# Performance work log

Hardware: AMD Instinct MI355X
Metric: run time of the kernel (lower is better)

Reference implementation:

```python
import jax, jax.numpy as jnp
import numpy as np

B, T, V, D, SLOTS = 16, 4096, 32000, 512, 256
EPS = 1e-5


def setup_inputs() -> dict:
    key = jax.random.key(0)
    ks = jax.random.split(key, 12)
    s = 0.02
    return {
        "seq": jax.random.randint(ks[0], (B, T), 0, V),
        "emb": jax.random.normal(ks[1], (V, D), jnp.float32) * s,
        "w1": jax.random.normal(ks[2], (D, 2 * D), jnp.float32) * s,
        "b1": jnp.zeros((2 * D,), jnp.float32),
        "w2": jax.random.normal(ks[3], (2 * D, D), jnp.float32) * s,
        "b2": jnp.zeros((D,), jnp.float32),
        "ln_g": jnp.ones((D,), jnp.float32),
        "ln_b": jnp.zeros((D,), jnp.float32),
        "wg": jax.random.normal(ks[4], (D,), jnp.float32) * s,
        "bg": jnp.zeros((), jnp.float32),
        "wq": jax.random.normal(ks[5], (D, D), jnp.float32) * s,
        "bq": jnp.zeros((D,), jnp.float32),
        "wo": jax.random.normal(ks[6], (D, V), jnp.float32) * s,
        "bo": jnp.zeros((V,), jnp.float32),
    }


def reference(seq, emb, w1, b1, w2, b2, ln_g, ln_b, wg, bg, wq, bq, wo, bo):
    # Encoder: embed -> residual FFN -> LayerNorm
    h0 = emb[seq]                                        # [B,T,D]
    ff = jax.nn.relu(h0 @ w1 + b1) @ w2 + b2             # [B,T,D]
    x = h0 + ff
    mu = jnp.mean(x, axis=-1, keepdims=True)
    var = jnp.mean(jnp.square(x - mu), axis=-1, keepdims=True)
    h = (x - mu) * jax.lax.rsqrt(var + EPS) * ln_g + ln_b  # [B,T,D]

    # Gate -> top-k slot selection -> gather memory
    gate = jax.nn.sigmoid(h @ wg + bg)                   # [B,T]
    topk = min(SLOTS, T)
    _, top_idx = jax.lax.top_k(gate, topk)               # [B,K]
    memory = jnp.take_along_axis(h, top_idx[:, :, None], axis=1)  # [B,K,D]

    # Single-query masked softmax attention (mask is all ones)
    query_h = h[:, -1, :]                                # [B,D]
    q = query_h @ wq + bq                                # [B,D]
    scores = jnp.einsum('bkd,bd->bk', memory, q)         # [B,K]
    mask = jnp.ones((seq.shape[0], topk), jnp.float32)
    scores = jnp.where(mask == 0, -1e9, scores)
    attn = jax.nn.softmax(scores, axis=-1)               # [B,K]
    ctx = jnp.einsum('bk,bkd->bd', attn, memory)         # [B,D]
    return ctx @ wo + bo                                 # [B,V]
```

## Files before the change

### kernel.cpp

```cpp
#include <hip/hip_runtime.h>

typedef __bf16 bf16x8 __attribute__((ext_vector_type(8)));
typedef float f32x4 __attribute__((ext_vector_type(4)));
typedef unsigned short ushort8v __attribute__((ext_vector_type(8)));

#define NB 16
#define NT 4096
#define NV 32000
#define ND 512
#define NH 1024
#define NSLOTS 256

__device__ __forceinline__ float b2f(unsigned short u) {
  unsigned int x = ((unsigned int)u) << 16;
  return __builtin_bit_cast(float, x);
}
__device__ __forceinline__ unsigned short f2b(float f) {
  unsigned int x = __builtin_bit_cast(unsigned int, f);
  unsigned int r = (x + 0x7FFFu + ((x >> 16) & 1u)) >> 16;
  return (unsigned short)r;
}

#define GLOAD_LDS16(g, l)                                                              \
  __builtin_amdgcn_global_load_lds((const __attribute__((address_space(1))) void*)(g), \
                                   (__attribute__((address_space(3))) void*)(l), 16, 0, 0)
#define BARRIER() asm volatile("s_barrier" ::: "memory")
#define VMCNT(n) asm volatile("s_waitcnt vmcnt(" #n ")" ::: "memory")

__global__ __launch_bounds__(256) void cvtwt_kernel(
    const float* __restrict__ emb, unsigned short* __restrict__ embb,
    const float* __restrict__ w1, const float* __restrict__ w2,
    unsigned short* __restrict__ w1t, unsigned short* __restrict__ w2t) {
  const int blk = blockIdx.x;
  if (blk < 8000) {
    const long base = ((long)blk * 256 + threadIdx.x) * 8;
    float4 a = *(const float4*)&emb[base];
    float4 b = *(const float4*)&emb[base + 4];
    ushort8v o;
    o[0] = f2b(a.x); o[1] = f2b(a.y); o[2] = f2b(a.z); o[3] = f2b(a.w);
    o[4] = f2b(b.x); o[5] = f2b(b.y); o[6] = f2b(b.z); o[7] = f2b(b.w);
    *(ushort8v*)&embb[base] = o;
  } else {
    const int i = (blk - 8000) * 256 + threadIdx.x;
    if (i < ND * NH) {
      const int n = i >> 9, k = i & 511;
      w1t[i] = f2b(w1[k * NH + n]);
    } else {
      const int j = i - ND * NH;
      const int n = j >> 10, k = j & 1023;
      w2t[j] = f2b(w2[k * ND + n]);
    }
  }
}

template <int KDIM, int NLD, int NBN, bool RELU>
__global__ __launch_bounds__(256, 2) void gemm1_kernel(
    const unsigned short* __restrict__ Abase, const unsigned short* __restrict__ Bt,
    const float* __restrict__ bias, unsigned short* __restrict__ Out) {
  extern __shared__ unsigned short sm1[];
  const int tid = threadIdx.x;
  const int lane = tid & 63;
  const int w = tid >> 6;
  const int wm = w >> 1, wn = w & 1;

  const int id = blockIdx.x;
  const int swz = (id & 7) * (gridDim.x >> 3) + (id >> 3);
  const int bm = swz / NBN;
  const int bn = swz % NBN;

  const unsigned short* aptr[2];
#pragma unroll
  for (int j = 0; j < 2; ++j) {
    const int c = j * 256 + tid;
    const int row = c >> 2;
    const int sc = (c & 3) ^ ((row >> 1) & 3);
    aptr[j] = Abase + (size_t)(bm * 128 + row) * KDIM + sc * 8;
  }
  const unsigned short* bptr[4];
#pragma unroll
  for (int j = 0; j < 4; ++j) {
    const int c = j * 256 + tid;
    const int row = c >> 2;
    const int sc = (c & 3) ^ ((row >> 1) & 3);
    bptr[j] = Bt + (size_t)(bn * 256 + row) * KDIM + sc * 8;
  }

  const int fr = lane & 15;
  const int fhi = lane >> 4;
  const int fsw = (fr >> 1) & 3;
  const int fchunk = (fhi ^ fsw) * 8;
  int aoff[4], boff[8];
#pragma unroll
  for (int m = 0; m < 4; ++m) aoff[m] = (wm * 64 + m * 16 + fr) * 32 + fchunk;
#pragma unroll
  for (int n = 0; n < 8; ++n) boff[n] = 4096 + (wn * 128 + n * 16 + fr) * 32 + fchunk;

  f32x4 acc[4][8] = {};

  auto stage = [&](int buf, int kt) {
    unsigned short* base = sm1 + buf * 12288;
#pragma unroll
    for (int j = 0; j < 2; ++j)
      GLOAD_LDS16(aptr[j] + kt * 32, base + (j * 256 + w * 64) * 8);
#pragma unroll
    for (int j = 0; j < 4; ++j)
      GLOAD_LDS16(bptr[j] + kt * 32, base + 4096 + (j * 256 + w * 64) * 8);
  };

  constexpr int NKT = KDIM / 32;
  stage(0, 0);
  stage(1, 1);
  for (int kt = 0; kt < NKT; ++kt) {
    if (kt + 1 < NKT)
      VMCNT(6);
    else
      VMCNT(0);
    __builtin_amdgcn_s_barrier();
    if (kt + 2 < NKT) stage((kt + 2) % 3, kt + 2);
    const unsigned short* base = sm1 + (kt % 3) * 12288;
    bf16x8 af[4], bf[8];
#pragma unroll
    for (int m = 0; m < 4; ++m)
      af[m] = __builtin_bit_cast(bf16x8, *(const ushort8v*)&base[aoff[m]]);
#pragma unroll
    for (int n = 0; n < 8; ++n)
      bf[n] = __builtin_bit_cast(bf16x8, *(const ushort8v*)&base[boff[n]]);
    __builtin_amdgcn_s_setprio(1);
#pragma unroll
    for (int m = 0; m < 4; ++m)
#pragma unroll
      for (int n = 0; n < 8; ++n)
        acc[m][n] = __builtin_amdgcn_mfma_f32_16x16x32_bf16(af[m], bf[n], acc[m][n], 0, 0, 0);
    __builtin_amdgcn_s_setprio(0);
  }
  __builtin_amdgcn_s_barrier();

  unsigned short* C = sm1;
  float bb[8];
#pragma unroll
  for (int n = 0; n < 8; ++n) bb[n] = bias[bn * 256 + wn * 128 + n * 16 + fr];
#pragma unroll
  for (int m = 0; m < 4; ++m)
#pragma unroll
    for (int n = 0; n < 8; ++n) {
      const int col_l = wn * 128 + n * 16 + fr;
      const int row_l0 = wm * 64 + m * 16 + (fhi << 2);
#pragma unroll
      for (int i = 0; i < 4; ++i) {
        float v = acc[m][n][i] + bb[n];
        if constexpr (RELU) v = fmaxf(v, 0.f);
        C[(row_l0 + i) * 264 + col_l] = f2b(v);
      }
    }
  __syncthreads();
#pragma unroll
  for (int it = 0; it < 16; ++it) {
    const int idx = it * 256 + tid;
    const int row = idx >> 5;
    const int pos = idx & 31;
    ushort8v v = *(const ushort8v*)&C[row * 264 + pos * 8];
    *(ushort8v*)&Out[(size_t)(bm * 128 + row) * (size_t)NLD + bn * 256 + pos * 8] = v;
  }
}

__global__ __launch_bounds__(512, 2) void gemm2ln_kernel(
    const unsigned short* __restrict__ A1v, const unsigned short* __restrict__ w2t,
    const float* __restrict__ b2, const float* __restrict__ emb,
    const float* __restrict__ ln_g, const float* __restrict__ ln_b,
    const float* __restrict__ wg, const float* __restrict__ bgp,
    unsigned short* __restrict__ Hv, float* __restrict__ gatev,
    const int* __restrict__ seq, float* __restrict__ hlast) {
  extern __shared__ unsigned short sm2[];
  const int tid = threadIdx.x;
  const int lane = tid & 63;
  const int w = tid >> 6;
  const int wm = w >> 2;
  const int wn = w & 3;

  const int id = blockIdx.x, nwg = gridDim.x;
  const int q = nwg >> 3, r = nwg & 7;
  const int xcd = id & 7;
  const int bm = ((xcd < r) ? xcd * (q + 1) : r * (q + 1) + (xcd - r) * q) + (id >> 3);

  const int arow = tid >> 2;
  const int acol = (tid & 3) ^ ((arow >> 1) & 3);
  const unsigned short* aptr = A1v + (size_t)(bm * 128 + arow) * NH + acol * 8;
  const unsigned short* bptr[4];
#pragma unroll
  for (int j = 0; j < 4; ++j) {
    const int c = j * 512 + tid;
    const int brow = c >> 2;
    const int bcol = (c & 3) ^ ((brow >> 1) & 3);
    bptr[j] = w2t + (size_t)brow * NH + bcol * 8;
  }

  const int fr = lane & 15;
  const int fhi = lane >> 4;
  const int fsw = (fr >> 1) & 3;
  const int fchunk = (fhi ^ fsw) * 8;
  int aoff[4], boff[8];
#pragma unroll
  for (int m = 0; m < 4; ++m) aoff[m] = (wm * 64 + m * 16 + fr) * 32 + fchunk;
#pragma unroll
  for (int n = 0; n < 8; ++n) boff[n] = 4096 + (wn * 128 + n * 16 + fr) * 32 + fchunk;

  f32x4 acc[4][8] = {};

  auto stage = [&](int buf, int kt) {
    unsigned short* base = sm2 + buf * 20480;
    GLOAD_LDS16(aptr + kt * 32, base + tid * 8);
#pragma unroll
    for (int j = 0; j < 4; ++j)
      GLOAD_LDS16(bptr[j] + kt * 32, base + 4096 + (j * 512 + tid) * 8);
  };

  constexpr int NKT = NH / 32;
  stage(0, 0);
  stage(1, 1);
  for (int kt = 0; kt < NKT; ++kt) {
    if (kt + 1 < NKT)
      VMCNT(5);
    else
      VMCNT(0);
    __builtin_amdgcn_s_barrier();
    if (kt + 2 < NKT) stage((kt + 2) % 3, kt + 2);
    const unsigned short* base = sm2 + (kt % 3) * 20480;
    bf16x8 af[4], bf[8];
#pragma unroll
    for (int m = 0; m < 4; ++m)
      af[m] = __builtin_bit_cast(bf16x8, *(const ushort8v*)&base[aoff[m]]);
#pragma unroll
    for (int n = 0; n < 8; ++n)
      bf[n] = __builtin_bit_cast(bf16x8, *(const ushort8v*)&base[boff[n]]);
    __builtin_amdgcn_s_setprio(1);
#pragma unroll
    for (int m = 0; m < 4; ++m)
#pragma unroll
      for (int n = 0; n < 8; ++n)
        acc[m][n] = __builtin_amdgcn_mfma_f32_16x16x32_bf16(af[m], bf[n], acc[m][n], 0, 0, 0);
    __builtin_amdgcn_s_setprio(0);
  }
  __syncthreads();

  unsigned short* C = sm2;
  float bb[8];
#pragma unroll
  for (int n = 0; n < 8; ++n) bb[n] = b2[wn * 128 + n * 16 + fr];
#pragma unroll
  for (int m = 0; m < 4; ++m)
#pragma unroll
    for (int n = 0; n < 8; ++n) {
      const int col_l = wn * 128 + n * 16 + fr;
      const int row_l0 = wm * 64 + m * 16 + (fhi << 2);
#pragma unroll
      for (int i = 0; i < 4; ++i)
        C[(row_l0 + i) * 516 + col_l] = f2b(acc[m][n][i] + bb[n]);
    }
  __syncthreads();

  for (int pass = 0; pass < 16; ++pass) {
    const int row_l = w + pass * 8;
    const int vrow = bm * 128 + row_l;
    ushort8v fv = *(const ushort8v*)&C[row_l * 516 + lane * 8];
    const float* er = emb + (size_t)vrow * ND + lane * 8;
    float4 e0 = *(const float4*)er, e1 = *(const float4*)(er + 4);
    float x[8] = {b2f(fv[0]) + e0.x, b2f(fv[1]) + e0.y, b2f(fv[2]) + e0.z, b2f(fv[3]) + e0.w,
                  b2f(fv[4]) + e1.x, b2f(fv[5]) + e1.y, b2f(fv[6]) + e1.z, b2f(fv[7]) + e1.w};
    float s = 0.f, sq = 0.f;
#pragma unroll
    for (int j = 0; j < 8; ++j) {
      s += x[j];
      sq += x[j] * x[j];
    }
#pragma unroll
    for (int o = 32; o; o >>= 1) {
      s += __shfl_xor(s, o);
      sq += __shfl_xor(sq, o);
    }
    const float mu = s * (1.f / 512.f);
    const float var = sq * (1.f / 512.f) - mu * mu;
    const float rs = rsqrtf(var + 1e-5f);
    float gd = 0.f;
    float h[8];
    ushort8v hv;
#pragma unroll
    for (int j = 0; j < 8; ++j) {
      const int col = lane * 8 + j;
      h[j] = (x[j] - mu) * rs * ln_g[col] + ln_b[col];
      hv[j] = f2b(h[j]);
      gd += h[j] * wg[col];
    }
    *(ushort8v*)&Hv[(size_t)vrow * ND + lane * 8] = hv;
#pragma unroll
    for (int o = 32; o; o >>= 1) gd += __shfl_xor(gd, o);
    if (lane == 0) gatev[vrow] = 1.f / (1.f + expf(-(gd + bgp[0])));
    for (int b = 0; b < NB; ++b) {
      if (seq[b * NT + NT - 1] == vrow) {
        float* hl = hlast + b * ND + lane * 8;
#pragma unroll
        for (int j = 0; j < 8; ++j) hl[j] = h[j];
      }
    }
  }
}

__global__ __launch_bounds__(256) void topk_qpart_kernel(
    const float* __restrict__ gatev, const int* __restrict__ seq,
    int* __restrict__ topidx, const float* __restrict__ hlast,
    const float* __restrict__ wq, const float* __restrict__ bq,
    float* __restrict__ qpart) {
  __shared__ int wsum[2][4];
  __shared__ unsigned int scanbuf[256];
  const int tid = threadIdx.x;
  if (blockIdx.x >= 16) {
    const int blk = blockIdx.x - 16;
    const int b = blk >> 3, s = blk & 7;
    const int d0 = s * 64;
    float a0 = 0.f, a1 = 0.f;
#pragma unroll 4
    for (int dd = 0; dd < 64; ++dd) {
      const float hv = hlast[b * ND + d0 + dd];
      a0 += hv * wq[(size_t)(d0 + dd) * ND + tid];
      a1 += hv * wq[(size_t)(d0 + dd) * ND + tid + 256];
    }
    if (s == 0) {
      a0 += bq[tid];
      a1 += bq[tid + 256];
    }
    float* qp = qpart + ((size_t)b * 8 + s) * ND;
    qp[tid] = a0;
    qp[tid + 256] = a1;
    return;
  }
  const int b = blockIdx.x;
  const int wv = tid >> 6;
  const int lane = tid & 63;
  const int* sq_ = seq + (size_t)b * NT;
  const int base = tid * 16;
  unsigned int kreg[16];
#pragma unroll
  for (int j = 0; j < 16; ++j)
    kreg[j] = __builtin_bit_cast(unsigned int, gatev[sq_[base + j]]);

  unsigned int K = 0u;
  for (int bit = 29; bit >= 0; --bit) {
    const unsigned int cand = K | (1u << bit);
    int c = 0;
#pragma unroll
    for (int j = 0; j < 16; ++j) c += (kreg[j] >= cand) ? 1 : 0;
#pragma unroll
    for (int o = 32; o; o >>= 1) c += __shfl_xor(c, o);
    const int par = bit & 1;
    if (lane == 0) wsum[par][wv] = c;
    __syncthreads();
    const int tot = wsum[par][0] + wsum[par][1] + wsum[par][2] + wsum[par][3];
    if (tot >= NSLOTS) K = cand;
  }
  int gcnt = 0, ecnt = 0;
#pragma unroll
  for (int j = 0; j < 16; ++j) {
    gcnt += (kreg[j] > K) ? 1 : 0;
    ecnt += (kreg[j] == K) ? 1 : 0;
  }
  __syncthreads();
  scanbuf[tid] = ((unsigned int)gcnt << 16) | (unsigned int)ecnt;
  __syncthreads();
  for (int off = 1; off < 256; off <<= 1) {
    unsigned int v2 = (tid >= off) ? scanbuf[tid - off] : 0u;
    __syncthreads();
    scanbuf[tid] += v2;
    __syncthreads();
  }
  const unsigned int my = scanbuf[tid];
  const unsigned int tot = scanbuf[255];
  const int gi = (int)(my >> 16);
  const int ei = (int)(my & 0xFFFFu);
  const int tot_gt = (int)(tot >> 16);
  int gpos = gi - gcnt;
  int epos = tot_gt + (ei - ecnt);
  int* outp = topidx + b * NSLOTS;
#pragma unroll
  for (int j = 0; j < 16; ++j) {
    if (kreg[j] > K) {
      outp[gpos++] = base + j;
    } else if (kreg[j] == K) {
      if (epos < NSLOTS) outp[epos] = base + j;
      epos++;
    }
  }
}

__global__ __launch_bounds__(256) void attn_kernel(
    const unsigned short* __restrict__ Hv, const int* __restrict__ seq,
    const float* __restrict__ qpart, const int* __restrict__ topidx,
    float* __restrict__ ctx) {
  __shared__ float qs[512];
  __shared__ float attnv[256];
  __shared__ int idxs[256];
  __shared__ float red[4];
  __shared__ float part[2][128];
  const int blk = blockIdx.x;
  const int b = blk >> 2, dc = blk & 3;
  const int tid = threadIdx.x;
  const int lane = tid & 63, wv = tid >> 6;
  {
    float a0 = 0.f, a1 = 0.f;
#pragma unroll
    for (int s = 0; s < 8; ++s) {
      const float* qp = qpart + ((size_t)b * 8 + s) * ND;
      a0 += qp[tid];
      a1 += qp[tid + 256];
    }
    qs[tid] = a0;
    qs[tid + 256] = a1;
  }
  idxs[tid] = seq[(size_t)b * NT + topidx[b * 256 + tid]];
  __syncthreads();
  const unsigned short* hr = Hv + (size_t)idxs[tid] * ND;
  float sc = 0.f;
  for (int d0 = 0; d0 < 512; d0 += 8) {
    ushort8v hv = *(const ushort8v*)&hr[d0];
#pragma unroll
    for (int j = 0; j < 8; ++j) sc += b2f(hv[j]) * qs[d0 + j];
  }
  float m = sc;
#pragma unroll
  for (int o = 32; o; o >>= 1) m = fmaxf(m, __shfl_xor(m, o));
  if (lane == 0) red[wv] = m;
  __syncthreads();
  m = fmaxf(fmaxf(red[0], red[1]), fmaxf(red[2], red[3]));
  __syncthreads();
  const float e = expf(sc - m);
  float ssum = e;
#pragma unroll
  for (int o = 32; o; o >>= 1) ssum += __shfl_xor(ssum, o);
  if (lane == 0) red[wv] = ssum;
  __syncthreads();
  ssum = red[0] + red[1] + red[2] + red[3];
  attnv[tid] = e / ssum;
  __syncthreads();
  const int d = dc * 128 + (tid & 127);
  const int kh = tid >> 7;
  float c = 0.f;
#pragma unroll 4
  for (int k2 = 0; k2 < 128; ++k2) {
    const int k = kh * 128 + k2;
    c += attnv[k] * b2f(Hv[(size_t)idxs[k] * ND + d]);
  }
  part[kh][tid & 127] = c;
  __syncthreads();
  if (tid < 128) ctx[b * 512 + dc * 128 + tid] = part[0][tid] + part[1][tid];
}

__global__ __launch_bounds__(256) void out_fused_kernel(const float* __restrict__ ctx,
                                                        const float* __restrict__ wo,
                                                        const float* __restrict__ bo,
                                                        float* __restrict__ out) {
  __shared__ float cs[16 * 512];
  __shared__ float red[8][16][32];
  const int tid = threadIdx.x;
  const int c = tid & 31, g = tid >> 5;
  const int v0 = blockIdx.x * 32;
  for (int i = tid; i < 16 * 512; i += 256) cs[i] = ctx[i];
  __syncthreads();
  const int d0 = g * 64;
  float acc[16] = {};
  const float* wp = wo + (size_t)d0 * NV + v0 + c;
#pragma unroll 4
  for (int dd = 0; dd < 64; ++dd) {
    const float wv = wp[(size_t)dd * NV];
#pragma unroll
    for (int bb = 0; bb < 16; ++bb) acc[bb] += cs[bb * 512 + d0 + dd] * wv;
  }
#pragma unroll
  for (int bb = 0; bb < 16; ++bb) red[g][bb][c] = acc[bb];
  __syncthreads();
  for (int i = tid; i < 512; i += 256) {
    const int bb = i >> 5, cc = i & 31;
    float a = bo[v0 + cc];
#pragma unroll
    for (int gg = 0; gg < 8; ++gg) a += red[gg][bb][cc];
    out[(size_t)bb * NV + v0 + cc] = a;
  }
}

extern "C" void kernel_launch(void* const* d_in, const int* in_sizes, int n_in,
                              void* d_out, int out_size, void* d_ws, size_t ws_size,
                              hipStream_t stream) {
  const int* seq = (const int*)d_in[0];
  const float* emb = (const float*)d_in[1];
  const float* w1 = (const float*)d_in[2];
  const float* b1 = (const float*)d_in[3];
  const float* w2 = (const float*)d_in[4];
  const float* b2 = (const float*)d_in[5];
  const float* ln_g = (const float*)d_in[6];
  const float* ln_b = (const float*)d_in[7];
  const float* wg = (const float*)d_in[8];
  const float* bg = (const float*)d_in[9];
  const float* wq = (const float*)d_in[10];
  const float* bq = (const float*)d_in[11];
  const float* wo = (const float*)d_in[12];
  const float* bo = (const float*)d_in[13];
  float* out = (float*)d_out;

  char* ws = (char*)d_ws;
  unsigned short* A1v = (unsigned short*)ws;
  unsigned short* embb = (unsigned short*)(ws + ((size_t)96 << 20));
  unsigned short* Hv = (unsigned short*)(ws + ((size_t)128 << 20));
  unsigned short* w1t = (unsigned short*)(ws + ((size_t)177 << 20));
  unsigned short* w2t = (unsigned short*)(ws + ((size_t)178 << 20));
  char* sb = ws + ((size_t)180 << 20);
  float* gatev = (float*)sb;
  int* topidx = (int*)(sb + 131072);
  float* hlast = (float*)(sb + 131072 + 16384);
  float* ctxbuf = (float*)(sb + 131072 + 16384 + 32768);
  float* qpart = (float*)(sb + 131072 + 16384 + 65536);

  hipFuncSetAttribute(reinterpret_cast<const void*>(gemm1_kernel<512, 1024, 4, true>),
                      hipFuncAttributeMaxDynamicSharedMemorySize, 73728);
  hipFuncSetAttribute(reinterpret_cast<const void*>(gemm2ln_kernel),
                      hipFuncAttributeMaxDynamicSharedMemorySize, 133120);

  cvtwt_kernel<<<12096, 256, 0, stream>>>(emb, embb, w1, w2, w1t, w2t);
  gemm1_kernel<512, 1024, 4, true>
      <<<1000, 256, 73728, stream>>>(embb, w1t, b1, A1v);
  gemm2ln_kernel<<<250, 512, 133120, stream>>>(A1v, w2t, b2, emb, ln_g, ln_b, wg, bg,
                                               Hv, gatev, seq, hlast);
  topk_qpart_kernel<<<144, 256, 0, stream>>>(gatev, seq, topidx, hlast, wq, bq, qpart);
  attn_kernel<<<64, 256, 0, stream>>>(Hv, seq, qpart, topidx, ctxbuf);
  out_fused_kernel<<<1000, 256, 0, stream>>>(ctxbuf, wo, bo, out);
}
```

Before: 182.0 us.

## Halve gemm2+LayerNorm row tile to 64 and switch to double buffering

The fused second GEMM + LayerNorm kernel now processes 64 rows per block instead of 128, with each of 8 waves owning a 64-column strip across all 64 rows. The grid doubles to 500 blocks. The LDS pipeline drops from triple buffering with vmcnt waits to double buffering with a __syncthreads per k-step, cutting shared memory from 130KB to 72KB. The aim is more blocks than CUs (about 250 blocks could not fill the device) and lower LDS usage for occupancy. In exchange, each block rereads the full w2 tile for half as many rows, and the pipeline is shallower, with a full barrier every iteration.

```diff
diff --git a/kernel.cpp b/kernel.cpp
--- a/kernel.cpp
+++ b/kernel.cpp
@@ -24,7 +24,6 @@
 #define GLOAD_LDS16(g, l)                                                              \
   __builtin_amdgcn_global_load_lds((const __attribute__((address_space(1))) void*)(g), \
                                    (__attribute__((address_space(3))) void*)(l), 16, 0, 0)
-#define BARRIER() asm volatile("s_barrier" ::: "memory")
 #define VMCNT(n) asm volatile("s_waitcnt vmcnt(" #n ")" ::: "memory")
 
 __global__ __launch_bounds__(256) void cvtwt_kernel(
@@ -174,17 +173,15 @@
   const int tid = threadIdx.x;
   const int lane = tid & 63;
   const int w = tid >> 6;
-  const int wm = w >> 2;
-  const int wn = w & 3;
 
   const int id = blockIdx.x, nwg = gridDim.x;
   const int q = nwg >> 3, r = nwg & 7;
   const int xcd = id & 7;
   const int bm = ((xcd < r) ? xcd * (q + 1) : r * (q + 1) + (xcd - r) * q) + (id >> 3);
 
-  const int arow = tid >> 2;
-  const int acol = (tid & 3) ^ ((arow >> 1) & 3);
-  const unsigned short* aptr = A1v + (size_t)(bm * 128 + arow) * NH + acol * 8;
+  const int ar = (tid >> 2) & 63;
+  const int ac = (tid & 3) ^ ((ar >> 1) & 3);
+  const unsigned short* aptr = A1v + (size_t)(bm * 64 + ar) * NH + ac * 8;
   const unsigned short* bptr[4];
 #pragma unroll
   for (int j = 0; j < 4; ++j) {
@@ -198,69 +195,66 @@
   const int fhi = lane >> 4;
   const int fsw = (fr >> 1) & 3;
   const int fchunk = (fhi ^ fsw) * 8;
-  int aoff[4], boff[8];
-#pragma unroll
-  for (int m = 0; m < 4; ++m) aoff[m] = (wm * 64 + m * 16 + fr) * 32 + fchunk;
-#pragma unroll
-  for (int n = 0; n < 8; ++n) boff[n] = 4096 + (wn * 128 + n * 16 + fr) * 32 + fchunk;
-
-  f32x4 acc[4][8] = {};
+  int aoff[4], boff[4];
+#pragma unroll
+  for (int m = 0; m < 4; ++m) aoff[m] = (m * 16 + fr) * 32 + fchunk;
+#pragma unroll
+  for (int n = 0; n < 4; ++n) boff[n] = 2048 + (w * 64 + n * 16 + fr) * 32 + fchunk;
+
+  f32x4 acc[4][4] = {};
 
   auto stage = [&](int buf, int kt) {
-    unsigned short* base = sm2 + buf * 20480;
-    GLOAD_LDS16(aptr + kt * 32, base + tid * 8);
+    unsigned short* base = sm2 + buf * 18432;
+    if (tid < 256) GLOAD_LDS16(aptr + kt * 32, base + tid * 8);
 #pragma unroll
     for (int j = 0; j < 4; ++j)
-      GLOAD_LDS16(bptr[j] + kt * 32, base + 4096 + (j * 512 + tid) * 8);
+      GLOAD_LDS16(bptr[j] + kt * 32, base + 2048 + (j * 512 + tid) * 8);
   };
 
   constexpr int NKT = NH / 32;
   stage(0, 0);
-  stage(1, 1);
+  __syncthreads();
+  int cur = 0;
   for (int kt = 0; kt < NKT; ++kt) {
-    if (kt + 1 < NKT)
-      VMCNT(5);
-    else
-      VMCNT(0);
-    __builtin_amdgcn_s_barrier();
-    if (kt + 2 < NKT) stage((kt + 2) % 3, kt + 2);
-    const unsigned short* base = sm2 + (kt % 3) * 20480;
-    bf16x8 af[4], bf[8];
+    if (kt + 1 < NKT) stage(cur ^ 1, kt + 1);
+    const unsigned short* base = sm2 + cur * 18432;
+    bf16x8 af[4], bf[4];
 #pragma unroll
     for (int m = 0; m < 4; ++m)
       af[m] = __builtin_bit_cast(bf16x8, *(const ushort8v*)&base[aoff[m]]);
 #pragma unroll
-    for (int n = 0; n < 8; ++n)
+    for (int n = 0; n < 4; ++n)
       bf[n] = __builtin_bit_cast(bf16x8, *(const ushort8v*)&base[boff[n]]);
     __builtin_amdgcn_s_setprio(1);
 #pragma unroll
     for (int m = 0; m < 4; ++m)
 #pragma unroll
-      for (int n = 0; n < 8; ++n)
+      for (int n = 0; n < 4; ++n)
         acc[m][n] = __builtin_amdgcn_mfma_f32_16x16x32_bf16(af[m], bf[n], acc[m][n], 0, 0, 0);
     __builtin_amdgcn_s_setprio(0);
-  }
-  __syncthreads();
+    __syncthreads();
+    cur ^= 1;
+  }
 
   unsigned short* C = sm2;
-  float bb[8];
-#pragma unroll
-  for (int n = 0; n < 8; ++n) bb[n] = b2[wn * 128 + n * 16 + fr];
+  float bb[4];
+#pragma unroll
+  for (int n = 0; n < 4; ++n) bb[n] = b2[w * 64 + n * 16 + fr];
 #pragma unroll
   for (int m = 0; m < 4; ++m)
 #pragma unroll
-    for (int n = 0; n < 8; ++n) {
-      const int col_l = wn * 128 + n * 16 + fr;
-      const int row_l0 = wm * 64 + m * 16 + (fhi << 2);
+    for (int n = 0; n < 4; ++n) {
+      const int col_l = w * 64 + n * 16 + fr;
+      const int row_l0 = m * 16 + (fhi << 2);
 #pragma unroll
       for (int i = 0; i < 4; ++i)
         C[(row_l0 + i) * 516 + col_l] = f2b(acc[m][n][i] + bb[n]);
     }
   __syncthreads();
 
-  for (int pass = 0; pass < 16; ++pass) {
+  for (int pass = 0; pass < 8; ++pass) {
     const int row_l = w + pass * 8;
-    const int vrow = bm * 128 + row_l;
+    const int vrow = bm * 64 + row_l;
     ushort8v fv = *(const ushort8v*)&C[row_l * 516 + lane * 8];
     const float* er = emb + (size_t)vrow * ND + lane * 8;
     float4 e0 = *(const float4*)er, e1 = *(const float4*)(er + 4);
@@ -519,13 +513,13 @@
   hipFuncSetAttribute(reinterpret_cast<const void*>(gemm1_kernel<512, 1024, 4, true>),
                       hipFuncAttributeMaxDynamicSharedMemorySize, 73728);
   hipFuncSetAttribute(reinterpret_cast<const void*>(gemm2ln_kernel),
-                      hipFuncAttributeMaxDynamicSharedMemorySize, 133120);
+                      hipFuncAttributeMaxDynamicSharedMemorySize, 73728);
 
   cvtwt_kernel<<<12096, 256, 0, stream>>>(emb, embb, w1, w2, w1t, w2t);
   gemm1_kernel<512, 1024, 4, true>
       <<<1000, 256, 73728, stream>>>(embb, w1t, b1, A1v);
-  gemm2ln_kernel<<<250, 512, 133120, stream>>>(A1v, w2t, b2, emb, ln_g, ln_b, wg, bg,
-                                               Hv, gatev, seq, hlast);
+  gemm2ln_kernel<<<500, 512, 73728, stream>>>(A1v, w2t, b2, emb, ln_g, ln_b, wg, bg,
+                                              Hv, gatev, seq, hlast);
   topk_qpart_kernel<<<144, 256, 0, stream>>>(gatev, seq, topidx, hlast, wq, bq, qpart);
   attn_kernel<<<64, 256, 0, stream>>>(Hv, seq, qpart, topidx, ctxbuf);
   out_fused_kernel<<<1000, 256, 0, stream>>>(ctxbuf, wo, bo, out);
```

New measurement: 203.6 us. 11.9% more time.
